# Optimization experiments

Measured on AMD Instinct MI355X. Metric: run time of the kernel, lower is better.

Reference implementation:

```python
import jax, jax.numpy as jnp
import numpy as np

C, PE, L, HEADS = 256, 64, 6, 4
N_GRAPHS, S = 2048, 64            # uniform graphs of S nodes -> dense batch is a reshape
N = N_GRAPHS * S                  # 131072 nodes
E = N * 4                         # 524288 edges
BN_EPS = 1e-5


def _bn(h, g, b):
    # BatchNorm1d, training-mode statistics (biased variance), affine
    m = h.mean(0)
    v = h.var(0)
    return (h - m) / jnp.sqrt(v + BN_EPS) * g + b


def setup_inputs() -> dict:
    key = jax.random.key(0)
    ks = iter(jax.random.split(key, 64))
    def rn(shape, scale=0.05):
        return jax.random.normal(next(ks), shape, dtype=jnp.float32) * scale
    x = jax.random.randint(next(ks), (N, 1), 0, 28)
    pe = jax.random.normal(next(ks), (N, 20), dtype=jnp.float32)
    epg = E // N_GRAPHS
    base = (jnp.arange(E) // epg) * S          # edges stay within their graph
    src = base + jax.random.randint(next(ks), (E,), 0, S)
    dst = base + jax.random.randint(next(ks), (E,), 0, S)
    edge_index = jnp.stack([src, dst])
    edge_attr = jax.random.randint(next(ks), (E,), 0, 4)
    batch = jnp.arange(N) // S
    return dict(
        x=x, pe=pe, edge_index=edge_index, edge_attr=edge_attr, batch=batch,
        node_emb=rn((28, C - PE), 1.0), pe_lin_w=rn((20, PE)), pe_lin_b=jnp.zeros(PE),
        pe_norm_g=jnp.ones(20), pe_norm_b=jnp.zeros(20),
        edge_emb=rn((4, C), 1.0),
        conv_w1=rn((L, C, C)), conv_b1=jnp.zeros((L, C)),
        conv_w2=rn((L, C, C)), conv_b2=jnp.zeros((L, C)),
        attn_in_w=rn((L, C, 3 * C)), attn_in_b=jnp.zeros((L, 3 * C)),
        attn_out_w=rn((L, C, C)), attn_out_b=jnp.zeros((L, C)),
        bn1_g=jnp.ones((L, C)), bn1_b=jnp.zeros((L, C)),
        bn2_g=jnp.ones((L, C)), bn2_b=jnp.zeros((L, C)),
        bn3_g=jnp.ones((L, C)), bn3_b=jnp.zeros((L, C)),
        mlp_w1=rn((L, C, 2 * C)), mlp_b1=jnp.zeros((L, 2 * C)),
        mlp_w2=rn((L, 2 * C, C)), mlp_b2=jnp.zeros((L, C)),
        head_w1=rn((C, C // 2)), head_b1=jnp.zeros(C // 2),
        head_w2=rn((C // 2, C // 4)), head_b2=jnp.zeros(C // 4),
        head_w3=rn((C // 4, 1)), head_b3=jnp.zeros(1),
    )


def reference(x, pe, edge_index, edge_attr, batch, node_emb, pe_lin_w, pe_lin_b,
              pe_norm_g, pe_norm_b, edge_emb, conv_w1, conv_b1, conv_w2, conv_b2,
              attn_in_w, attn_in_b, attn_out_w, attn_out_b,
              bn1_g, bn1_b, bn2_g, bn2_b, bn3_g, bn3_b,
              mlp_w1, mlp_b1, mlp_w2, mlp_b2,
              head_w1, head_b1, head_w2, head_b2, head_w3, head_b3):
    x_pe = _bn(pe, pe_norm_g, pe_norm_b)
    h = jnp.concatenate([node_emb[x[:, 0]], x_pe @ pe_lin_w + pe_lin_b], axis=1)  # [N, C]
    ea = edge_emb[edge_attr]                                                      # [E, C]
    src, dst = edge_index[0], edge_index[1]
    d = C // HEADS
    scale = 1.0 / jnp.sqrt(jnp.float32(d))
    for l in range(L):
        # --- local GINEConv: nn((1+eps)*x_i + sum_j relu(x_j + e_ij)), eps=0 ---
        msg = jax.nn.relu(h[src] + ea)                          # gather + add + relu
        aggr = jax.ops.segment_sum(msg, dst, num_segments=N)    # scatter-add
        z = h + aggr
        hl = jax.nn.relu(z @ conv_w1[l] + conv_b1[l]) @ conv_w2[l] + conv_b2[l]
        hl = _bn(hl + h, bn1_g[l], bn1_b[l])                    # residual + norm1
        # --- global multihead attention on dense batch [G, S, C] ---
        hd = h.reshape(N_GRAPHS, S, C)
        qkv = hd @ attn_in_w[l] + attn_in_b[l]
        q, k, v = jnp.split(qkv, 3, axis=-1)
        q = q.reshape(N_GRAPHS, S, HEADS, d).transpose(0, 2, 1, 3)
        k = k.reshape(N_GRAPHS, S, HEADS, d).transpose(0, 2, 1, 3)
        v = v.reshape(N_GRAPHS, S, HEADS, d).transpose(0, 2, 1, 3)
        a = jax.nn.softmax(jnp.einsum('ghqd,ghkd->ghqk', q, k) * scale, axis=-1)
        o = jnp.einsum('ghqk,ghkd->ghqd', a, v).transpose(0, 2, 1, 3).reshape(N_GRAPHS, S, C)
        o = (o @ attn_out_w[l] + attn_out_b[l]).reshape(N, C)
        ha = _bn(o + h, bn2_g[l], bn2_b[l])                     # residual + norm2
        # --- combine + FFN ---
        out = hl + ha
        ff = jax.nn.relu(out @ mlp_w1[l] + mlp_b1[l]) @ mlp_w2[l] + mlp_b2[l]
        h = _bn(out + ff, bn3_g[l], bn3_b[l])                   # residual + norm3
    pooled = jax.ops.segment_sum(h, batch, num_segments=N_GRAPHS)  # global_add_pool -> [G, C]
    t = jax.nn.relu(pooled @ head_w1 + head_b1)
    t = jax.nn.relu(t @ head_w2 + head_b2)
    return t @ head_w3 + head_b3                                   # [G, 1]
```

## Files before the change

kernel.cpp:

```cpp
#include <hip/hip_runtime.h>

#define N_NODES 131072
#define N_EDGES 524288
#define CCH 256
#define N_GRAPHS_ 2048
#define SEQ 64
#define LAYERS 6

typedef unsigned short US;
typedef __attribute__((ext_vector_type(8))) short v8s;
typedef __attribute__((ext_vector_type(8))) unsigned short v8us;
typedef __attribute__((ext_vector_type(4))) float v4f;

__device__ __forceinline__ float b2f(US u) { return __uint_as_float(((unsigned)u) << 16); }
__device__ __forceinline__ US f2b(float f) {
    unsigned u = __float_as_uint(f);
    return (US)((u + 0x7fff + ((u >> 16) & 1)) >> 16);
}

__device__ float g_stats[512];
__device__ float g_aff1[512];
__device__ float g_aff2[512];
__device__ float g_aff3[512];
__device__ float g_pe[40];
__device__ float g_peaff[40];
__device__ US    g_wt[6 * 655360];
__device__ int   g_csr[N_EDGES];
__device__ int   g_off[N_GRAPHS_ * 65];

__global__ __launch_bounds__(256) void wt_k(const float* __restrict__ cw1, const float* __restrict__ cw2,
                                            const float* __restrict__ aiw, const float* __restrict__ aow,
                                            const float* __restrict__ mw1, const float* __restrict__ mw2) {
    __shared__ float t[64][65];
    int b = blockIdx.x;
    int l = b / 160, r = b % 160;
    const float* src; int ldw, ldk, ctiles; size_t doff;
    if (r < 16)      { src = cw1 + (size_t)l * 65536;  ldw = 256; ldk = 256; ctiles = 4;  doff = 0;      }
    else if (r < 32) { src = cw2 + (size_t)l * 65536;  ldw = 256; ldk = 256; ctiles = 4;  doff = 65536;  r -= 16; }
    else if (r < 80) { src = aiw + (size_t)l * 196608; ldw = 768; ldk = 256; ctiles = 12; doff = 131072; r -= 32; }
    else if (r < 96) { src = aow + (size_t)l * 65536;  ldw = 256; ldk = 256; ctiles = 4;  doff = 327680; r -= 80; }
    else if (r < 128){ src = mw1 + (size_t)l * 131072; ldw = 512; ldk = 256; ctiles = 8;  doff = 393216; r -= 96; }
    else             { src = mw2 + (size_t)l * 131072; ldw = 256; ldk = 512; ctiles = 4;  doff = 524288; r -= 128; }
    int kt = r / ctiles, ct = r % ctiles;
    int k0 = kt * 64, c0 = ct * 64;
    US* dst = g_wt + (size_t)l * 655360 + doff;
    int tid = threadIdx.x;
    int rr = tid >> 4, c4 = (tid & 15) * 4;
    #pragma unroll
    for (int j = 0; j < 4; j++) {
        float4 v = *(const float4*)(src + (size_t)(k0 + rr + j * 16) * ldw + c0 + c4);
        t[rr + j * 16][c4 + 0] = v.x; t[rr + j * 16][c4 + 1] = v.y;
        t[rr + j * 16][c4 + 2] = v.z; t[rr + j * 16][c4 + 3] = v.w;
    }
    __syncthreads();
    #pragma unroll
    for (int j = 0; j < 4; j++) {
        int crow = rr + j * 16;
        ushort4 o;
        o.x = f2b(t[c4 + 0][crow]); o.y = f2b(t[c4 + 1][crow]);
        o.z = f2b(t[c4 + 2][crow]); o.w = f2b(t[c4 + 3][crow]);
        *(ushort4*)(dst + (size_t)(c0 + crow) * ldk + k0 + c4) = o;
    }
}

__global__ __launch_bounds__(256) void csr_k(const int* __restrict__ ei,
                                             const int* __restrict__ attr) {
    __shared__ int deg[64], off[65];
    int g = blockIdx.x, tid = threadIdx.x;
    if (tid < 64) deg[tid] = 0;
    __syncthreads();
    int e = g * 256 + tid;
    int d = ei[N_EDGES + e] - g * 64;
    int slot = atomicAdd(&deg[d], 1);
    __syncthreads();
    if (tid == 0) {
        off[0] = 0;
        for (int i = 0; i < 64; i++) off[i + 1] = off[i] + deg[i];
    }
    __syncthreads();
    g_csr[g * 256 + off[d] + slot] = (ei[e] - g * 64) | (attr[e] << 6);
    if (tid < 65) g_off[g * 65 + tid] = off[tid];
}

__global__ __launch_bounds__(256) void pe_part_k(const float* __restrict__ pe) {
    __shared__ float red[240], red2[240];
    int b = blockIdx.x, tid = threadIdx.x;
    float s = 0.f, s2 = 0.f;
    if (tid < 240) {
        int ch = tid % 20, sub = tid / 20;
        size_t r0 = (size_t)b * 512;
        for (int r = sub; r < 512; r += 12) {
            float v = pe[(r0 + r) * 20 + ch];
            s += v; s2 += v * v;
        }
        red[tid] = s; red2[tid] = s2;
    }
    __syncthreads();
    if (tid < 20) {
        float ts = 0.f, ts2 = 0.f;
        #pragma unroll
        for (int sub = 0; sub < 12; sub++) { ts += red[sub * 20 + tid]; ts2 += red2[sub * 20 + tid]; }
        atomicAdd(&g_pe[tid], ts);
        atomicAdd(&g_pe[20 + tid], ts2);
    }
}

__global__ __launch_bounds__(64) void pe_fin_k(const float* __restrict__ g,
                                               const float* __restrict__ b) {
    int t = threadIdx.x;
    if (t < 20) {
        float mean = g_pe[t] / (float)N_NODES;
        float var  = g_pe[20 + t] / (float)N_NODES - mean * mean;
        float a = g[t] * rsqrtf(var + 1e-5f);
        g_peaff[t] = a;
        g_peaff[20 + t] = b[t] - mean * a;
        g_pe[t] = 0.f;
        g_pe[20 + t] = 0.f;
    }
}

__global__ __launch_bounds__(256) void embed_k(const int* __restrict__ x,
                                               const float* __restrict__ pe,
                                               const float* __restrict__ node_emb,
                                               const float* __restrict__ plw,
                                               const float* __restrict__ plb,
                                               US* __restrict__ h) {
    int n = blockIdx.x;
    int tid = threadIdx.x;
    int xi = x[n];
    float v;
    if (tid < 192) {
        v = node_emb[xi * 192 + tid];
    } else {
        int j = tid - 192;
        float s = plb[j];
        #pragma unroll
        for (int k = 0; k < 20; k++) {
            float p = pe[(size_t)n * 20 + k] * g_peaff[k] + g_peaff[20 + k];
            s += p * plw[k * 64 + j];
        }
        v = s;
    }
    h[(size_t)n * CCH + tid] = f2b(v);
}

__global__ __launch_bounds__(256) void aggr_z_k(const US* __restrict__ h,
                                                const float* __restrict__ eemb,
                                                US* __restrict__ z) {
    __shared__ US ht[64 * 264];
    __shared__ float em[4 * 260];
    __shared__ int off[65], ce[256];
    int g = blockIdx.x, tid = threadIdx.x;
    for (int v = tid; v < 2048; v += 256) {
        int row = v >> 5, seg = (v & 31) * 8;
        *(v8us*)&ht[row * 264 + seg] = *(const v8us*)(h + (size_t)(g * 64 + row) * 256 + seg);
    }
    for (int i = tid; i < 1024; i += 256)
        em[(i >> 8) * 260 + (i & 255)] = eemb[(i >> 8) * 256 + (i & 255)];
    ce[tid] = g_csr[g * 256 + tid];
    if (tid < 65) off[tid] = g_off[g * 65 + tid];
    __syncthreads();

    int dst = tid >> 2, cq = (tid & 3) * 4;
    float acc[64];
    #pragma unroll
    for (int i = 0; i < 64; i++) acc[i] = 0.f;
    int e1 = off[dst + 1];
    for (int e = off[dst]; e < e1; e++) {
        int val = ce[e];
        int src = val & 63, a = (val >> 6) & 3;
        #pragma unroll
        for (int i = 0; i < 16; i++) {
            int c = cq + i * 16;
            ushort4 hv = *(ushort4*)&ht[src * 264 + c];
            float4 ev = *(float4*)&em[a * 260 + c];
            acc[i * 4 + 0] += fmaxf(b2f(hv.x) + ev.x, 0.f);
            acc[i * 4 + 1] += fmaxf(b2f(hv.y) + ev.y, 0.f);
            acc[i * 4 + 2] += fmaxf(b2f(hv.z) + ev.z, 0.f);
            acc[i * 4 + 3] += fmaxf(b2f(hv.w) + ev.w, 0.f);
        }
    }
    US* zp = z + (size_t)(g * 64 + dst) * 256;
    #pragma unroll
    for (int i = 0; i < 16; i++) {
        int c = cq + i * 16;
        ushort4 hv = *(ushort4*)&ht[dst * 264 + c];
        ushort4 o;
        o.x = f2b(b2f(hv.x) + acc[i * 4 + 0]);
        o.y = f2b(b2f(hv.y) + acc[i * 4 + 1]);
        o.z = f2b(b2f(hv.z) + acc[i * 4 + 2]);
        o.w = f2b(b2f(hv.w) + acc[i * 4 + 3]);
        *(ushort4*)(zp + c) = o;
    }
}

template<int NG>
__global__ __launch_bounds__(256, 2) void gemm_mfma_k(const US* __restrict__ A,
                                                      size_t woff, int ldk,
                                                      int w0, int w1, int w2, int w3,
                                                      const float* __restrict__ bias,
                                                      const US* __restrict__ res,
                                                      US* __restrict__ Y, int mode) {
    const US* __restrict__ Wt = g_wt + woff;
    __shared__ __align__(16) US As[128 * 40];
    __shared__ __align__(16) US Bs[NG * 64 * 40];
    int tid = threadIdx.x;
    size_t row0 = (size_t)blockIdx.x * 128;
    int w = tid >> 6, l = tid & 63;

    int a_off0 = (w * 32 + (l & 15)) * 40 + (l >> 4) * 8;
    int a_off1 = a_off0 + 16 * 40;
    int b_off  = (l & 15) * 40 + (l >> 4) * 8;
    int sb_c = tid >> 2, sb_ko = (tid & 3) * 8;

    v4f acc[2][NG * 4];
    #pragma unroll
    for (int i = 0; i < 2; i++)
        #pragma unroll
        for (int t = 0; t < NG * 4; t++) acc[i][t] = (v4f){0.f, 0.f, 0.f, 0.f};

    for (int k0 = 0; k0 < 256; k0 += 32) {
        #pragma unroll
        for (int p = 0; p < 2; p++) {
            int cidx = tid + p * 256;
            int row = cidx >> 2, ko = (cidx & 3) * 8;
            *(v8us*)&As[row * 40 + ko] = *(const v8us*)(A + (row0 + row) * 256 + k0 + ko);
        }
        #pragma unroll
        for (int p = 0; p < NG; p++) {
            int wb = (p == 0) ? w0 : (p == 1) ? w1 : (p == 2) ? w2 : w3;
            *(v8us*)&Bs[(p * 64 + sb_c) * 40 + sb_ko] =
                *(const v8us*)(Wt + (size_t)(wb + sb_c) * ldk + k0 + sb_ko);
        }
        __syncthreads();
        v8s a0 = *(v8s*)&As[a_off0];
        v8s a1 = *(v8s*)&As[a_off1];
        #pragma unroll
        for (int t = 0; t < NG * 4; t++) {
            v8s bf = *(v8s*)&Bs[b_off + t * 640];
            acc[0][t] = __builtin_amdgcn_mfma_f32_16x16x32_bf16(a0, bf, acc[0][t], 0, 0, 0);
            acc[1][t] = __builtin_amdgcn_mfma_f32_16x16x32_bf16(a1, bf, acc[1][t], 0, 0, 0);
        }
        __syncthreads();
    }
    int col_l = l & 15;
    int rs = (l >> 4) * 4;
    #pragma unroll
    for (int i = 0; i < 2; i++) {
        #pragma unroll
        for (int t = 0; t < NG * 4; t++) {
            int grp = t >> 2;
            int wb = (grp == 0) ? w0 : (grp == 1) ? w1 : (grp == 2) ? w2 : w3;
            int c = t * 16 + col_l;
            float bv = bias ? bias[wb + (t & 3) * 16 + col_l] : 0.f;
            #pragma unroll
            for (int r = 0; r < 4; r++) {
                size_t rr = row0 + w * 32 + i * 16 + rs + r;
                float v = acc[i][t][r] + bv;
                if (mode == 1) v = fmaxf(v, 0.f);
                if (mode == 2) v += b2f(res[rr * 256 + c]);
                Y[rr * 256 + c] = f2b(v);
            }
        }
    }
}

__global__ __launch_bounds__(64) void attn_k(const US* __restrict__ qkv,
                                             US* __restrict__ o) {
    __shared__ __align__(16) US Ps[64 * 72];
    __shared__ __align__(16) US Vt[64 * 72];
    int g = blockIdx.x, l = threadIdx.x;
    int li = l & 15, hi8 = (l >> 4) * 8, hi4 = (l >> 4) * 4;
    const US* base = qkv + (size_t)g * 64 * 256;

    {
        v8us vv[8];
        #pragma unroll
        for (int jv = 0; jv < 8; jv++)
            vv[jv] = *(const v8us*)(base + l * 256 + 128 + jv * 8);
        #pragma unroll
        for (int jv = 0; jv < 8; jv++)
            #pragma unroll
            for (int e = 0; e < 8; e++)
                Vt[(jv * 8 + e) * 72 + l] = vv[jv][e];
    }

    v8s Qf[4][2], Kf[4][2];
    #pragma unroll
    for (int t = 0; t < 4; t++)
        #pragma unroll
        for (int ds = 0; ds < 2; ds++) {
            Qf[t][ds] = *(const v8s*)(base + (t * 16 + li) * 256 + ds * 32 + hi8);
            Kf[t][ds] = *(const v8s*)(base + (t * 16 + li) * 256 + 64 + ds * 32 + hi8);
        }

    v4f S[4][4];
    #pragma unroll
    for (int qt = 0; qt < 4; qt++)
        #pragma unroll
        for (int kt = 0; kt < 4; kt++) {
            v4f a = (v4f){0.f, 0.f, 0.f, 0.f};
            a = __builtin_amdgcn_mfma_f32_16x16x32_bf16(Qf[qt][0], Kf[kt][0], a, 0, 0, 0);
            a = __builtin_amdgcn_mfma_f32_16x16x32_bf16(Qf[qt][1], Kf[kt][1], a, 0, 0, 0);
            S[qt][kt] = a;
        }

    #pragma unroll
    for (int qt = 0; qt < 4; qt++)
        #pragma unroll
        for (int r = 0; r < 4; r++) {
            float mx = -1e30f;
            #pragma unroll
            for (int kt = 0; kt < 4; kt++) {
                S[qt][kt][r] *= 0.125f;
                mx = fmaxf(mx, S[qt][kt][r]);
            }
            mx = fmaxf(mx, __shfl_xor(mx, 1));
            mx = fmaxf(mx, __shfl_xor(mx, 2));
            mx = fmaxf(mx, __shfl_xor(mx, 4));
            mx = fmaxf(mx, __shfl_xor(mx, 8));
            float sum = 0.f;
            #pragma unroll
            for (int kt = 0; kt < 4; kt++) {
                float e = __expf(S[qt][kt][r] - mx);
                S[qt][kt][r] = e;
                sum += e;
            }
            sum += __shfl_xor(sum, 1);
            sum += __shfl_xor(sum, 2);
            sum += __shfl_xor(sum, 4);
            sum += __shfl_xor(sum, 8);
            float inv = 1.f / sum;
            #pragma unroll
            for (int kt = 0; kt < 4; kt++)
                Ps[(qt * 16 + hi4 + r) * 72 + kt * 16 + li] = f2b(S[qt][kt][r] * inv);
        }

    v4f O[4][4];
    #pragma unroll
    for (int qt = 0; qt < 4; qt++)
        #pragma unroll
        for (int jt = 0; jt < 4; jt++) O[qt][jt] = (v4f){0.f, 0.f, 0.f, 0.f};
    #pragma unroll
    for (int ks = 0; ks < 2; ks++) {
        v8s Pf[4], Vf[4];
        #pragma unroll
        for (int qt = 0; qt < 4; qt++)
            Pf[qt] = *(v8s*)&Ps[(qt * 16 + li) * 72 + ks * 32 + hi8];
        #pragma unroll
        for (int jt = 0; jt < 4; jt++)
            Vf[jt] = *(v8s*)&Vt[(jt * 16 + li) * 72 + ks * 32 + hi8];
        #pragma unroll
        for (int qt = 0; qt < 4; qt++)
            #pragma unroll
            for (int jt = 0; jt < 4; jt++)
                O[qt][jt] = __builtin_amdgcn_mfma_f32_16x16x32_bf16(Pf[qt], Vf[jt], O[qt][jt], 0, 0, 0);
    }

    #pragma unroll
    for (int qt = 0; qt < 4; qt++)
        #pragma unroll
        for (int jt = 0; jt < 4; jt++)
            #pragma unroll
            for (int r = 0; r < 4; r++)
                Ps[(qt * 16 + hi4 + r) * 72 + jt * 16 + li] = f2b(O[qt][jt][r]);
    US* ob = o + (size_t)(g * 64 + l) * 256;
    #pragma unroll
    for (int jv = 0; jv < 8; jv++)
        *(v8us*)(ob + jv * 8) = *(v8us*)&Ps[l * 72 + jv * 8];
}

__global__ __launch_bounds__(256) void stats_k(const US* __restrict__ Y) {
    int c = threadIdx.x;
    size_t r0 = (size_t)blockIdx.x * 1024;
    float s = 0.f, s2 = 0.f;
    for (int r = 0; r < 1024; r++) {
        float v = b2f(Y[(r0 + r) * CCH + c]);
        s += v; s2 += v * v;
    }
    atomicAdd(&g_stats[c], s);
    atomicAdd(&g_stats[CCH + c], s2);
}

__global__ __launch_bounds__(256) void affine_k(const float* __restrict__ g,
                                                const float* __restrict__ b, int sel) {
    int c = threadIdx.x;
    float mean = g_stats[c] / (float)N_NODES;
    float var  = g_stats[CCH + c] / (float)N_NODES - mean * mean;
    float a = g[c] * rsqrtf(var + 1e-5f);
    float* dst = (sel == 0) ? g_aff1 : (sel == 1) ? g_aff2 : g_aff3;
    dst[c] = a;
    dst[CCH + c] = b[c] - mean * a;
    g_stats[c] = 0.f;
    g_stats[CCH + c] = 0.f;
}

__global__ __launch_bounds__(256) void combine_k(const US* __restrict__ y1,
                                                 const US* __restrict__ y2,
                                                 US* __restrict__ out) {
    size_t idx = (size_t)blockIdx.x * 256 + threadIdx.x;
    size_t stride = (size_t)gridDim.x * 256;
    for (; idx < (size_t)N_NODES * CCH / 8; idx += stride) {
        size_t i = idx * 8;
        int c = (int)(i & 255);
        v8us a = *(const v8us*)(y1 + i);
        v8us b = *(const v8us*)(y2 + i);
        v8us o;
        #pragma unroll
        for (int j = 0; j < 8; j++) {
            float v = b2f(a[j]) * g_aff1[c + j] + g_aff1[CCH + c + j] +
                      b2f(b[j]) * g_aff2[c + j] + g_aff2[CCH + c + j];
            o[j] = f2b(v);
        }
        *(v8us*)(out + i) = o;
    }
}

__global__ __launch_bounds__(256) void apply_k(US* __restrict__ h) {
    size_t idx = (size_t)blockIdx.x * 256 + threadIdx.x;
    size_t stride = (size_t)gridDim.x * 256;
    for (; idx < (size_t)N_NODES * CCH / 8; idx += stride) {
        size_t i = idx * 8;
        int c = (int)(i & 255);
        v8us a = *(const v8us*)(h + i);
        v8us o;
        #pragma unroll
        for (int j = 0; j < 8; j++)
            o[j] = f2b(b2f(a[j]) * g_aff3[c + j] + g_aff3[CCH + c + j]);
        *(v8us*)(h + i) = o;
    }
}

__global__ __launch_bounds__(256) void pool_k(const US* __restrict__ h,
                                              float* __restrict__ pooled) {
    int g = blockIdx.x, c = threadIdx.x;
    float s = 0.f;
    for (int ss = 0; ss < SEQ; ss++) s += b2f(h[((size_t)g * SEQ + ss) * CCH + c]);
    pooled[(size_t)g * CCH + c] = s;
}

__global__ __launch_bounds__(128) void head_k(const float* __restrict__ pooled,
                                              const float* __restrict__ w1, const float* __restrict__ b1,
                                              const float* __restrict__ w2, const float* __restrict__ b2,
                                              const float* __restrict__ w3, const float* __restrict__ b3,
                                              float* __restrict__ outp) {
    __shared__ float p[256], t1[128], t2[64];
    int g = blockIdx.x, tid = threadIdx.x;
    p[tid] = pooled[(size_t)g * CCH + tid];
    p[tid + 128] = pooled[(size_t)g * CCH + 128 + tid];
    __syncthreads();
    float s = b1[tid];
    for (int k = 0; k < 256; k++) s += p[k] * w1[k * 128 + tid];
    t1[tid] = fmaxf(s, 0.f);
    __syncthreads();
    if (tid < 64) {
        float s2 = b2[tid];
        for (int k = 0; k < 128; k++) s2 += t1[k] * w2[k * 64 + tid];
        t2[tid] = fmaxf(s2, 0.f);
    }
    __syncthreads();
    if (tid == 0) {
        float s3 = b3[0];
        for (int k = 0; k < 64; k++) s3 += t2[k] * w3[k];
        outp[g] = s3;
    }
}

extern "C" void kernel_launch(void* const* d_in, const int* in_sizes, int n_in,
                              void* d_out, int out_size, void* d_ws, size_t ws_size,
                              hipStream_t stream) {
    const int*   x         = (const int*)  d_in[0];
    const float* pe        = (const float*)d_in[1];
    const int*   ei        = (const int*)  d_in[2];
    const int*   eattr     = (const int*)  d_in[3];
    const float* node_emb  = (const float*)d_in[5];
    const float* pe_lin_w  = (const float*)d_in[6];
    const float* pe_lin_b  = (const float*)d_in[7];
    const float* pe_norm_g = (const float*)d_in[8];
    const float* pe_norm_b = (const float*)d_in[9];
    const float* edge_emb  = (const float*)d_in[10];
    const float* conv_w1   = (const float*)d_in[11];
    const float* conv_b1   = (const float*)d_in[12];
    const float* conv_w2   = (const float*)d_in[13];
    const float* conv_b2   = (const float*)d_in[14];
    const float* attn_in_w = (const float*)d_in[15];
    const float* attn_in_b = (const float*)d_in[16];
    const float* attn_out_w= (const float*)d_in[17];
    const float* attn_out_b= (const float*)d_in[18];
    const float* bn1_g     = (const float*)d_in[19];
    const float* bn1_b     = (const float*)d_in[20];
    const float* bn2_g     = (const float*)d_in[21];
    const float* bn2_b     = (const float*)d_in[22];
    const float* bn3_g     = (const float*)d_in[23];
    const float* bn3_b     = (const float*)d_in[24];
    const float* mlp_w1    = (const float*)d_in[25];
    const float* mlp_b1    = (const float*)d_in[26];
    const float* mlp_w2    = (const float*)d_in[27];
    const float* mlp_b2    = (const float*)d_in[28];
    const float* head_w1   = (const float*)d_in[29];
    const float* head_b1   = (const float*)d_in[30];
    const float* head_w2   = (const float*)d_in[31];
    const float* head_b2   = (const float*)d_in[32];
    const float* head_w3   = (const float*)d_in[33];
    const float* head_b3   = (const float*)d_in[34];
    (void)in_sizes; (void)n_in; (void)out_size; (void)ws_size;

    char* ws = (char*)d_ws;
    US* h = (US*)(ws);
    US* A = (US*)(ws + 67108864ULL);
    US* B = (US*)(ws + 134217728ULL);
    US* C = (US*)(ws + 201326592ULL);
    float* pooled = (float*)(ws + 67108864ULL);

    wt_k<<<960, 256, 0, stream>>>(conv_w1, conv_w2, attn_in_w, attn_out_w, mlp_w1, mlp_w2);
    csr_k<<<N_GRAPHS_, 256, 0, stream>>>(ei, eattr);
    pe_part_k<<<256, 256, 0, stream>>>(pe);
    pe_fin_k<<<1, 64, 0, stream>>>(pe_norm_g, pe_norm_b);
    embed_k<<<N_NODES, 256, 0, stream>>>(x, pe, node_emb, pe_lin_w, pe_lin_b, h);

    for (int l = 0; l < LAYERS; l++) {
        size_t wl = (size_t)l * 655360;

        aggr_z_k<<<N_GRAPHS_, 256, 0, stream>>>(h, edge_emb, A);
        gemm_mfma_k<4><<<1024, 256, 0, stream>>>(A, wl, 256, 0, 64, 128, 192,
                                                 conv_b1 + l * 256, nullptr, B, 1);
        gemm_mfma_k<4><<<1024, 256, 0, stream>>>(B, wl + 65536, 256, 0, 64, 128, 192,
                                                 conv_b2 + l * 256, h, C, 2);
        stats_k<<<128, 256, 0, stream>>>(C);
        affine_k<<<1, 256, 0, stream>>>(bn1_g + l * 256, bn1_b + l * 256, 0);

        for (int hh = 0; hh < 4; hh++) {
            gemm_mfma_k<3><<<1024, 256, 0, stream>>>(h, wl + 131072, 256,
                                                     hh * 64, 256 + hh * 64, 512 + hh * 64, 0,
                                                     attn_in_b + l * 768, nullptr, A, 0);
            attn_k<<<N_GRAPHS_, 64, 0, stream>>>(A, B + hh * 64);
        }
        gemm_mfma_k<4><<<1024, 256, 0, stream>>>(B, wl + 327680, 256, 0, 64, 128, 192,
                                                 attn_out_b + l * 256, h, h, 2);
        stats_k<<<128, 256, 0, stream>>>(h);
        affine_k<<<1, 256, 0, stream>>>(bn2_g + l * 256, bn2_b + l * 256, 1);

        combine_k<<<2048, 256, 0, stream>>>(C, h, A);
        gemm_mfma_k<4><<<1024, 256, 0, stream>>>(A, wl + 393216, 256, 0, 64, 128, 192,
                                                 mlp_b1 + l * 512, nullptr, B, 1);
        gemm_mfma_k<4><<<1024, 256, 0, stream>>>(B, wl + 524288, 512, 0, 64, 128, 192,
                                                 mlp_b2 + l * 256, A, C, 2);
        gemm_mfma_k<4><<<1024, 256, 0, stream>>>(A, wl + 393216, 256, 256, 320, 384, 448,
                                                 mlp_b1 + l * 512, nullptr, B, 1);
        gemm_mfma_k<4><<<1024, 256, 0, stream>>>(B, wl + 524288 + 256, 512, 0, 64, 128, 192,
                                                 nullptr, C, h, 2);
        stats_k<<<128, 256, 0, stream>>>(h);
        affine_k<<<1, 256, 0, stream>>>(bn3_g + l * 256, bn3_b + l * 256, 2);
        apply_k<<<2048, 256, 0, stream>>>(h);
    }

    pool_k<<<N_GRAPHS_, 256, 0, stream>>>(h, pooled);
    head_k<<<N_GRAPHS_, 128, 0, stream>>>(pooled, head_w1, head_b1, head_w2, head_b2,
                                          head_w3, head_b3, (float*)d_out);
}
```

Measured before the change: 6.088 ms.

## Fuse BatchNorm statistics into GEMM epilogue and register-prefetch GEMM tiles

Removes the separate stats_k pass by accumulating per-column sum and sum of squares in the GEMM epilogue. The partial sums are reduced through wave shuffles and shared memory, then added into global stats with atomics. It also stages the next k-slice of A and W in registers before the MFMA loop so global loads overlap compute. This saves three full reads of the activation tensor per layer. The cost is extra registers and many more atomics, since 1024 blocks each issue 512, and fp32 accumulation order changes slightly.

```diff
diff --git a/kernel.cpp b/kernel.cpp
--- a/kernel.cpp
+++ b/kernel.cpp
@@ -194,7 +194,7 @@
     }
 }
 
-template<int NG>
+template<int NG, bool STATS>
 __global__ __launch_bounds__(256, 2) void gemm_mfma_k(const US* __restrict__ A,
                                                       size_t woff, int ldk,
                                                       int w0, int w1, int w2, int w3,
@@ -208,10 +208,13 @@
     size_t row0 = (size_t)blockIdx.x * 128;
     int w = tid >> 6, l = tid & 63;
 
+    int sb_c = tid >> 2, sb_ko = (tid & 3) * 8;
     int a_off0 = (w * 32 + (l & 15)) * 40 + (l >> 4) * 8;
     int a_off1 = a_off0 + 16 * 40;
     int b_off  = (l & 15) * 40 + (l >> 4) * 8;
-    int sb_c = tid >> 2, sb_ko = (tid & 3) * 8;
+
+    const US* aptr0 = A + (row0 + sb_c) * 256 + sb_ko;
+    const US* aptr1 = aptr0 + 64 * 256;
 
     v4f acc[2][NG * 4];
     #pragma unroll
@@ -219,20 +222,32 @@
         #pragma unroll
         for (int t = 0; t < NG * 4; t++) acc[i][t] = (v4f){0.f, 0.f, 0.f, 0.f};
 
-    for (int k0 = 0; k0 < 256; k0 += 32) {
-        #pragma unroll
-        for (int p = 0; p < 2; p++) {
-            int cidx = tid + p * 256;
-            int row = cidx >> 2, ko = (cidx & 3) * 8;
-            *(v8us*)&As[row * 40 + ko] = *(const v8us*)(A + (row0 + row) * 256 + k0 + ko);
-        }
-        #pragma unroll
-        for (int p = 0; p < NG; p++) {
-            int wb = (p == 0) ? w0 : (p == 1) ? w1 : (p == 2) ? w2 : w3;
-            *(v8us*)&Bs[(p * 64 + sb_c) * 40 + sb_ko] =
-                *(const v8us*)(Wt + (size_t)(wb + sb_c) * ldk + k0 + sb_ko);
-        }
+    v8us pa0 = *(const v8us*)aptr0;
+    v8us pa1 = *(const v8us*)aptr1;
+    v8us pb[NG];
+    #pragma unroll
+    for (int p = 0; p < NG; p++) {
+        int wb = (p == 0) ? w0 : (p == 1) ? w1 : (p == 2) ? w2 : w3;
+        pb[p] = *(const v8us*)(Wt + (size_t)(wb + sb_c) * ldk + sb_ko);
+    }
+
+    for (int kc = 0; kc < 8; kc++) {
+        *(v8us*)&As[sb_c * 40 + sb_ko] = pa0;
+        *(v8us*)&As[(sb_c + 64) * 40 + sb_ko] = pa1;
+        #pragma unroll
+        for (int p = 0; p < NG; p++)
+            *(v8us*)&Bs[(p * 64 + sb_c) * 40 + sb_ko] = pb[p];
         __syncthreads();
+        if (kc < 7) {
+            int kn = (kc + 1) * 32;
+            pa0 = *(const v8us*)(aptr0 + kn);
+            pa1 = *(const v8us*)(aptr1 + kn);
+            #pragma unroll
+            for (int p = 0; p < NG; p++) {
+                int wb = (p == 0) ? w0 : (p == 1) ? w1 : (p == 2) ? w2 : w3;
+                pb[p] = *(const v8us*)(Wt + (size_t)(wb + sb_c) * ldk + kn + sb_ko);
+            }
+        }
         v8s a0 = *(v8s*)&As[a_off0];
         v8s a1 = *(v8s*)&As[a_off1];
         #pragma unroll
@@ -243,8 +258,14 @@
         }
         __syncthreads();
     }
+
     int col_l = l & 15;
     int rs = (l >> 4) * 4;
+    float cs[NG * 4], cs2[NG * 4];
+    if (STATS) {
+        #pragma unroll
+        for (int t = 0; t < NG * 4; t++) { cs[t] = 0.f; cs2[t] = 0.f; }
+    }
     #pragma unroll
     for (int i = 0; i < 2; i++) {
         #pragma unroll
@@ -259,8 +280,32 @@
                 float v = acc[i][t][r] + bv;
                 if (mode == 1) v = fmaxf(v, 0.f);
                 if (mode == 2) v += b2f(res[rr * 256 + c]);
+                if (STATS) { cs[t] += v; cs2[t] += v * v; }
                 Y[rr * 256 + c] = f2b(v);
             }
+        }
+    }
+    if (STATS) {
+        #pragma unroll
+        for (int t = 0; t < NG * 4; t++) {
+            cs[t]  += __shfl_xor(cs[t], 16);  cs[t]  += __shfl_xor(cs[t], 32);
+            cs2[t] += __shfl_xor(cs2[t], 16); cs2[t] += __shfl_xor(cs2[t], 32);
+        }
+        float* sred = (float*)As;
+        if ((l >> 4) == 0) {
+            #pragma unroll
+            for (int t = 0; t < NG * 4; t++) {
+                sred[w * 256 + t * 16 + col_l] = cs[t];
+                sred[1024 + w * 256 + t * 16 + col_l] = cs2[t];
+            }
+        }
+        __syncthreads();
+        int c = tid;
+        if (c < NG * 64) {
+            float s  = sred[c] + sred[256 + c] + sred[512 + c] + sred[768 + c];
+            float s2 = sred[1024 + c] + sred[1280 + c] + sred[1536 + c] + sred[1792 + c];
+            atomicAdd(&g_stats[c], s);
+            atomicAdd(&g_stats[CCH + c], s2);
         }
     }
 }
@@ -368,18 +413,6 @@
     #pragma unroll
     for (int jv = 0; jv < 8; jv++)
         *(v8us*)(ob + jv * 8) = *(v8us*)&Ps[l * 72 + jv * 8];
-}
-
-__global__ __launch_bounds__(256) void stats_k(const US* __restrict__ Y) {
-    int c = threadIdx.x;
-    size_t r0 = (size_t)blockIdx.x * 1024;
-    float s = 0.f, s2 = 0.f;
-    for (int r = 0; r < 1024; r++) {
-        float v = b2f(Y[(r0 + r) * CCH + c]);
-        s += v; s2 += v * v;
-    }
-    atomicAdd(&g_stats[c], s);
-    atomicAdd(&g_stats[CCH + c], s2);
 }
 
 __global__ __launch_bounds__(256) void affine_k(const float* __restrict__ g,
@@ -522,34 +555,31 @@
         size_t wl = (size_t)l * 655360;
 
         aggr_z_k<<<N_GRAPHS_, 256, 0, stream>>>(h, edge_emb, A);
-        gemm_mfma_k<4><<<1024, 256, 0, stream>>>(A, wl, 256, 0, 64, 128, 192,
-                                                 conv_b1 + l * 256, nullptr, B, 1);
-        gemm_mfma_k<4><<<1024, 256, 0, stream>>>(B, wl + 65536, 256, 0, 64, 128, 192,
-                                                 conv_b2 + l * 256, h, C, 2);
-        stats_k<<<128, 256, 0, stream>>>(C);
+        gemm_mfma_k<4, false><<<1024, 256, 0, stream>>>(A, wl, 256, 0, 64, 128, 192,
+                                                        conv_b1 + l * 256, nullptr, B, 1);
+        gemm_mfma_k<4, true><<<1024, 256, 0, stream>>>(B, wl + 65536, 256, 0, 64, 128, 192,
+                                                       conv_b2 + l * 256, h, C, 2);
         affine_k<<<1, 256, 0, stream>>>(bn1_g + l * 256, bn1_b + l * 256, 0);
 
         for (int hh = 0; hh < 4; hh++) {
-            gemm_mfma_k<3><<<1024, 256, 0, stream>>>(h, wl + 131072, 256,
-                                                     hh * 64, 256 + hh * 64, 512 + hh * 64, 0,
-                                                     attn_in_b + l * 768, nullptr, A, 0);
+            gemm_mfma_k<3, false><<<1024, 256, 0, stream>>>(h, wl + 131072, 256,
+                                                            hh * 64, 256 + hh * 64, 512 + hh * 64, 0,
+                                                            attn_in_b + l * 768, nullptr, A, 0);
             attn_k<<<N_GRAPHS_, 64, 0, stream>>>(A, B + hh * 64);
         }
-        gemm_mfma_k<4><<<1024, 256, 0, stream>>>(B, wl + 327680, 256, 0, 64, 128, 192,
-                                                 attn_out_b + l * 256, h, h, 2);
-        stats_k<<<128, 256, 0, stream>>>(h);
+        gemm_mfma_k<4, true><<<1024, 256, 0, stream>>>(B, wl + 327680, 256, 0, 64, 128, 192,
+                                                       attn_out_b + l * 256, h, h, 2);
         affine_k<<<1, 256, 0, stream>>>(bn2_g + l * 256, bn2_b + l * 256, 1);
 
         combine_k<<<2048, 256, 0, stream>>>(C, h, A);
-        gemm_mfma_k<4><<<1024, 256, 0, stream>>>(A, wl + 393216, 256, 0, 64, 128, 192,
-                                                 mlp_b1 + l * 512, nullptr, B, 1);
-        gemm_mfma_k<4><<<1024, 256, 0, stream>>>(B, wl + 524288, 512, 0, 64, 128, 192,
-                                                 mlp_b2 + l * 256, A, C, 2);
-        gemm_mfma_k<4><<<1024, 256, 0, stream>>>(A, wl + 393216, 256, 256, 320, 384, 448,
-                                                 mlp_b1 + l * 512, nullptr, B, 1);
-        gemm_mfma_k<4><<<1024, 256, 0, stream>>>(B, wl + 524288 + 256, 512, 0, 64, 128, 192,
-                                                 nullptr, C, h, 2);
-        stats_k<<<128, 256, 0, stream>>>(h);
+        gemm_mfma_k<4, false><<<1024, 256, 0, stream>>>(A, wl + 393216, 256, 0, 64, 128, 192,
+                                                        mlp_b1 + l * 512, nullptr, B, 1);
+        gemm_mfma_k<4, false><<<1024, 256, 0, stream>>>(B, wl + 524288, 512, 0, 64, 128, 192,
+                                                        mlp_b2 + l * 256, A, C, 2);
+        gemm_mfma_k<4, false><<<1024, 256, 0, stream>>>(A, wl + 393216, 256, 256, 320, 384, 448,
+                                                        mlp_b1 + l * 512, nullptr, B, 1);
+        gemm_mfma_k<4, true><<<1024, 256, 0, stream>>>(B, wl + 524288 + 256, 512, 0, 64, 128, 192,
+                                                       nullptr, C, h, 2);
         affine_k<<<1, 256, 0, stream>>>(bn3_g + l * 256, bn3_b + l * 256, 2);
         apply_k<<<2048, 256, 0, stream>>>(h);
     }
```

Measured after the change: 5.743 ms. 5.7% less time.
